# Performance work log

Measured on AMD Instinct MI355X. Metric: run time of the kernel, lower is better.

Reference implementation:

```python
import jax, jax.numpy as jnp
import numpy as np

N_NODES = 40000
N_EDGES = 640000
IN, HID, OUT = 128, 256, 47


def setup_inputs() -> dict:
    key = jax.random.key(0)
    ks = jax.random.split(key, 8)
    x = jax.random.normal(ks[0], (N_NODES, IN), dtype=jnp.float32)
    # PyTorch Linear(fan_in, fan_out): store as [fan_in, fan_out] for y = h @ W + b
    W1 = jax.random.normal(ks[1], (2 * IN, HID), dtype=jnp.float32) / np.sqrt(2 * IN)
    b1 = jnp.zeros((HID,), jnp.float32)
    W2 = jax.random.normal(ks[2], (2 * HID, HID), dtype=jnp.float32) / np.sqrt(2 * HID)
    b2 = jnp.zeros((HID,), jnp.float32)
    W3 = jax.random.normal(ks[3], (2 * HID, OUT), dtype=jnp.float32) / np.sqrt(2 * HID)
    b3 = jnp.zeros((OUT,), jnp.float32)
    src = jax.random.randint(ks[4], (N_EDGES,), 0, N_NODES, dtype=jnp.int64 if jax.config.jax_enable_x64 else jnp.int32)
    dst = jax.random.randint(ks[5], (N_EDGES,), 0, N_NODES, dtype=jnp.int64 if jax.config.jax_enable_x64 else jnp.int32)
    return {"x": x, "W1": W1, "b1": b1, "W2": W2, "b2": b2, "W3": W3, "b3": b3,
            "src": src, "dst": dst}


def _sage_layer(h, src, dst, W, b):
    # copy_u -> mean: gather src features, scatter-sum into dst, divide by in-degree
    msum = jax.ops.segment_sum(h[src], dst, num_segments=N_NODES)  # [N, d]
    deg = jax.ops.segment_sum(jnp.ones_like(dst, dtype=h.dtype), dst, num_segments=N_NODES)
    mean = msum / jnp.maximum(deg, 1.0)[:, None]  # zero-degree nodes get 0 (DGL mean convention)
    cat = jnp.concatenate([h, mean], axis=1)      # [N, 2d]
    return cat @ W + b


def reference(x, W1, b1, W2, b2, W3, b3, src, dst):
    # dropout is identity in eval mode
    h = jax.nn.relu(_sage_layer(x, src, dst, W1, b1))
    h = jax.nn.relu(_sage_layer(h, src, dst, W2, b2))
    return _sage_layer(h, src, dst, W3, b3)
```

## Files before the change

kernel.cpp:

```cpp
#include <hip/hip_runtime.h>

#define NNODES 40000
#define NEDGES 640000
#define DIN 128
#define DHID 256
#define DOUT 47
#define NCNT 40960
#define NPART (NCNT / 256)

typedef __attribute__((ext_vector_type(8))) short short8;
typedef __attribute__((ext_vector_type(4))) float f32x4;

#define GLD16(gp, lp)                                                        \
    __builtin_amdgcn_global_load_lds(                                        \
        (const __attribute__((address_space(1))) void*)(gp),                 \
        (__attribute__((address_space(3))) void*)(lp), 16, 0, 0)

__device__ inline float bf2f(unsigned short u) {
    union { unsigned int i; float f; } c; c.i = ((unsigned int)u) << 16; return c.f;
}
__device__ inline unsigned short f2bf(float f) {
    union { float f; unsigned int i; } c; c.f = f;
    unsigned int x = c.i;
    x += 0x7fff + ((x >> 16) & 1);
    return (unsigned short)(x >> 16);
}

__global__ void hist_kernel(const int* __restrict__ dst, int* __restrict__ cnt) {
    int t = blockIdx.x * blockDim.x + threadIdx.x;
    if (t < NEDGES) atomicAdd(&cnt[dst[t]], 1);
}

__global__ void part_kernel(const int* __restrict__ cnt, int* __restrict__ part) {
    int b = blockIdx.x, t = threadIdx.x;
    int v = cnt[b * 256 + t];
#pragma unroll
    for (int off = 32; off > 0; off >>= 1) v += __shfl_down(v, off);
    __shared__ int ws[4];
    if ((t & 63) == 0) ws[t >> 6] = v;
    __syncthreads();
    if (t == 0) part[b] = ws[0] + ws[1] + ws[2] + ws[3];
}

__global__ void scanpart_kernel(const int* __restrict__ part, int* __restrict__ partoff) {
    __shared__ int sh[256];
    int t = threadIdx.x;
    int v = (t < NPART) ? part[t] : 0;
    sh[t] = v;
    __syncthreads();
    for (int off = 1; off < 256; off <<= 1) {
        int add = (t >= off) ? sh[t - off] : 0;
        __syncthreads();
        sh[t] += add;
        __syncthreads();
    }
    if (t < NPART) partoff[t] = sh[t] - v;
}

__global__ void writeptr_kernel(const int* __restrict__ cnt, const int* __restrict__ partoff,
                                int* __restrict__ rowptr) {
    __shared__ int sh[256];
    int b = blockIdx.x, t = threadIdx.x;
    int idx = b * 256 + t;
    int v = cnt[idx];
    sh[t] = v;
    __syncthreads();
    for (int off = 1; off < 256; off <<= 1) {
        int add = (t >= off) ? sh[t - off] : 0;
        __syncthreads();
        sh[t] += add;
        __syncthreads();
    }
    rowptr[idx] = partoff[b] + sh[t] - v;
}

__global__ void fill_kernel(const int* __restrict__ src, const int* __restrict__ dst,
                            const int* __restrict__ rowptr, int* __restrict__ fill,
                            unsigned short* __restrict__ eidx) {
    int e = blockIdx.x * blockDim.x + threadIdx.x;
    if (e < NEDGES) {
        int d = dst[e];
        int pos = rowptr[d] + atomicAdd(&fill[d], 1);
        eidx[pos] = (unsigned short)src[e];
    }
}

__global__ void conv_all_kernel(const float* __restrict__ x,
                                const float* __restrict__ W1,
                                const float* __restrict__ W2,
                                const float* __restrict__ W3,
                                unsigned short* __restrict__ xbf,
                                unsigned short* __restrict__ wt1,
                                unsigned short* __restrict__ wt2,
                                unsigned short* __restrict__ wt3) {
    const int N0 = NNODES * DIN / 4;
    const int N1 = 2 * DIN * DHID;
    const int N2 = 2 * DHID * DHID;
    const int N3 = 94 * 256;
    int t = blockIdx.x * blockDim.x + threadIdx.x;
    if (t < N0) {
        float4 v = ((const float4*)x)[t];
        ushort4 r;
        r.x = f2bf(v.x); r.y = f2bf(v.y); r.z = f2bf(v.z); r.w = f2bf(v.w);
        ((ushort4*)xbf)[t] = r;
    } else if (t < N0 + N1) {
        int u = t - N0;
        int k = u >> 8, n = u & 255;
        wt1[(size_t)n * 256 + k] = f2bf(W1[u]);
    } else if (t < N0 + N1 + N2) {
        int u = t - N0 - N1;
        int k = u >> 8, n = u & 255;
        wt2[(size_t)n * 512 + k] = f2bf(W2[u]);
    } else if (t < N0 + N1 + N2 + N3) {
        int u = t - N0 - N1 - N2;
        int n = u >> 8, k = u & 255;
        float v = (n < 47) ? W3[(size_t)k * DOUT + n]
                           : W3[(size_t)(k + DHID) * DOUT + (n - 47)];
        wt3[u] = f2bf(v);
    }
}

template <int D>
__global__ void agg_bf16_kernel(const unsigned short* __restrict__ h,
                                const int* __restrict__ rowptr,
                                const unsigned short* __restrict__ eidx,
                                unsigned short* __restrict__ mean) {
    constexpr int VPL = D / 64;
    const int node = blockIdx.x * (blockDim.x >> 6) + (threadIdx.x >> 6);
    if (node >= NNODES) return;
    const int lane = threadIdx.x & 63;
    const int beg = rowptr[node], end = rowptr[node + 1];
    const unsigned short* hp = h + lane * VPL;

    float acc[VPL];
#pragma unroll
    for (int i = 0; i < VPL; ++i) acc[i] = 0.0f;

    for (int base = beg; base < end; base += 64) {
        int n = min(64, end - base);
        int myidx = (base + lane < end) ? (int)eidx[base + lane] : 0;
        int j = 0;
        for (; j + 8 <= n; j += 8) {
            int s[8];
#pragma unroll
            for (int u = 0; u < 8; ++u) s[u] = __shfl(myidx, j + u);
            if constexpr (VPL == 4) {
                ushort4 v[8];
#pragma unroll
                for (int u = 0; u < 8; ++u) v[u] = *(const ushort4*)(hp + (size_t)s[u] * D);
#pragma unroll
                for (int u = 0; u < 8; ++u) {
                    acc[0] += bf2f(v[u].x); acc[1] += bf2f(v[u].y);
                    acc[2] += bf2f(v[u].z); acc[3] += bf2f(v[u].w);
                }
            } else {
                ushort2 v[8];
#pragma unroll
                for (int u = 0; u < 8; ++u) v[u] = *(const ushort2*)(hp + (size_t)s[u] * D);
#pragma unroll
                for (int u = 0; u < 8; ++u) {
                    acc[0] += bf2f(v[u].x); acc[1] += bf2f(v[u].y);
                }
            }
        }
        for (; j + 4 <= n; j += 4) {
            int s[4];
#pragma unroll
            for (int u = 0; u < 4; ++u) s[u] = __shfl(myidx, j + u);
            if constexpr (VPL == 4) {
                ushort4 v[4];
#pragma unroll
                for (int u = 0; u < 4; ++u) v[u] = *(const ushort4*)(hp + (size_t)s[u] * D);
#pragma unroll
                for (int u = 0; u < 4; ++u) {
                    acc[0] += bf2f(v[u].x); acc[1] += bf2f(v[u].y);
                    acc[2] += bf2f(v[u].z); acc[3] += bf2f(v[u].w);
                }
            } else {
                ushort2 v[4];
#pragma unroll
                for (int u = 0; u < 4; ++u) v[u] = *(const ushort2*)(hp + (size_t)s[u] * D);
#pragma unroll
                for (int u = 0; u < 4; ++u) {
                    acc[0] += bf2f(v[u].x); acc[1] += bf2f(v[u].y);
                }
            }
        }
        for (; j < n; ++j) {
            int s = __shfl(myidx, j);
            if constexpr (VPL == 4) {
                ushort4 v = *(const ushort4*)(hp + (size_t)s * D);
                acc[0] += bf2f(v.x); acc[1] += bf2f(v.y);
                acc[2] += bf2f(v.z); acc[3] += bf2f(v.w);
            } else {
                ushort2 v = *(const ushort2*)(hp + (size_t)s * D);
                acc[0] += bf2f(v.x); acc[1] += bf2f(v.y);
            }
        }
    }
    float inv = (end > beg) ? 1.0f / (float)(end - beg) : 0.0f;
    unsigned short* o = mean + (size_t)node * D + lane * VPL;
    if constexpr (VPL == 4) {
        ushort4 r;
        r.x = f2bf(acc[0] * inv); r.y = f2bf(acc[1] * inv);
        r.z = f2bf(acc[2] * inv); r.w = f2bf(acc[3] * inv);
        *(ushort4*)o = r;
    } else {
        ushort2 r;
        r.x = f2bf(acc[0] * inv); r.y = f2bf(acc[1] * inv);
        *(ushort2*)o = r;
    }
}

__global__ void agg_p_kernel(const unsigned short* __restrict__ P,
                             const int* __restrict__ rowptr,
                             const unsigned short* __restrict__ eidx,
                             float* __restrict__ out) {
    const int node = blockIdx.x * (blockDim.x >> 6) + (threadIdx.x >> 6);
    if (node >= NNODES) return;
    const int lane = threadIdx.x & 63;
    const int beg = rowptr[node], end = rowptr[node + 1];
    const bool active = lane < 48;
    const int lc = active ? lane : 0;

    float acc = 0.0f;
    for (int base = beg; base < end; base += 64) {
        int n = min(64, end - base);
        int myidx = (base + lane < end) ? (int)eidx[base + lane] : 0;
        int j = 0;
        for (; j + 4 <= n; j += 4) {
            int s0 = __shfl(myidx, j);
            int s1 = __shfl(myidx, j + 1);
            int s2 = __shfl(myidx, j + 2);
            int s3 = __shfl(myidx, j + 3);
            if (active) {
                float a = bf2f(P[(size_t)s0 * 48 + lc]) + bf2f(P[(size_t)s1 * 48 + lc]);
                float b = bf2f(P[(size_t)s2 * 48 + lc]) + bf2f(P[(size_t)s3 * 48 + lc]);
                acc += a + b;
            }
        }
        for (; j < n; ++j) {
            int s = __shfl(myidx, j);
            if (active) acc += bf2f(P[(size_t)s * 48 + lc]);
        }
    }
    if (lane < 47 && end > beg) {
        out[(size_t)node * DOUT + lane] += acc / (float)(end - beg);
    }
}

template <int D>
__launch_bounds__(256, 2)
__global__ void gemm_fused_kernel(const unsigned short* __restrict__ H,
                                  const unsigned short* __restrict__ Mn,
                                  const unsigned short* __restrict__ Wt,
                                  const float* __restrict__ bias,
                                  unsigned short* __restrict__ hout) {
    constexpr int K = 2 * D;
    __shared__ uint4 As4[64 * 4];
    __shared__ uint4 Bs4[256 * 4];

    const int tid = threadIdx.x;
    const int lane = tid & 63;
    const int w = tid >> 6;
    const int row0 = blockIdx.x * 64;

    const int lr = lane >> 2;
    const int lslot = lane & 3;
    const int arow = w * 16 + lr;
    const int aoff = (lslot ^ ((arow >> 1) & 3)) * 8;
    const size_t abase = (size_t)(row0 + arow) * D;

    f32x4 acc[4][4];
#pragma unroll
    for (int m = 0; m < 4; ++m)
#pragma unroll
        for (int n = 0; n < 4; ++n) {
            f32x4 z = {0.0f, 0.0f, 0.0f, 0.0f};
            acc[m][n] = z;
        }

    const int fr = lane & 15;
    const int sl = lane >> 4;

#pragma unroll
    for (int k0 = 0; k0 < K; k0 += 32) {
        {
            const unsigned short* ap = (k0 < D) ? (H + abase + k0 + aoff)
                                                : (Mn + abase + (k0 - D) + aoff);
            GLD16(ap, (char*)As4 + w * 1024);
        }
#pragma unroll
        for (int c = 0; c < 4; ++c) {
            int q = w * 4 + c;
            int brow = q * 16 + lr;
            const unsigned short* bp =
                Wt + (size_t)brow * K + k0 + ((lslot ^ ((brow >> 1) & 3)) * 8);
            GLD16(bp, (char*)Bs4 + q * 1024);
        }
        __syncthreads();

        short8 af[4], bfv[4];
#pragma unroll
        for (int m = 0; m < 4; ++m) {
            int r = m * 16 + fr;
            union { uint4 u; short8 s; } cc;
            cc.u = As4[r * 4 + (sl ^ ((r >> 1) & 3))];
            af[m] = cc.s;
        }
#pragma unroll
        for (int n = 0; n < 4; ++n) {
            int r = w * 64 + n * 16 + fr;
            union { uint4 u; short8 s; } cc;
            cc.u = Bs4[r * 4 + (sl ^ ((r >> 1) & 3))];
            bfv[n] = cc.s;
        }
#pragma unroll
        for (int m = 0; m < 4; ++m)
#pragma unroll
            for (int n = 0; n < 4; ++n)
                acc[m][n] = __builtin_amdgcn_mfma_f32_16x16x32_bf16(af[m], bfv[n], acc[m][n], 0, 0, 0);
        __syncthreads();
    }

#pragma unroll
    for (int m = 0; m < 4; ++m) {
#pragma unroll
        for (int n = 0; n < 4; ++n) {
            int col = w * 64 + n * 16 + fr;
            float bv = bias[col];
#pragma unroll
            for (int q = 0; q < 4; ++q) {
                int row = row0 + m * 16 + sl * 4 + q;
                float v = fmaxf(acc[m][n][q] + bv, 0.0f);
                hout[(size_t)row * 256 + col] = f2bf(v);
            }
        }
    }
}

__launch_bounds__(256, 2)
__global__ void gemm3_kernel(const unsigned short* __restrict__ H,
                             const unsigned short* __restrict__ Wt,
                             const float* __restrict__ bias,
                             float* __restrict__ outp,
                             unsigned short* __restrict__ Pout,
                             int d, int N) {
    const int K = 2 * d;
    __shared__ uint4 AsB[128 * 4];
    __shared__ uint4 BsB[128 * 4];

    const int tid = threadIdx.x;
    const int lane = tid & 63;
    const int wid = tid >> 6;
    const int wr = wid >> 1, wc = wid & 1;
    const int row0 = blockIdx.x * 128;

    const int sr = tid >> 1;
    const int sh = tid & 1;
    const int gar = min(row0 + sr, NNODES - 1);
    const int gbr = min(sr, N - 1);
    const int ssw = (sr >> 1) & 3;

    f32x4 acc[4][4];
#pragma unroll
    for (int m = 0; m < 4; ++m)
#pragma unroll
        for (int n = 0; n < 4; ++n) {
            f32x4 z = {0.0f, 0.0f, 0.0f, 0.0f};
            acc[m][n] = z;
        }

    for (int k0 = 0; k0 < K; k0 += 32) {
        {
            const unsigned short* p = H + (size_t)gar * K + k0 + sh * 16;
            uint4 v0 = *(const uint4*)p;
            uint4 v1 = *(const uint4*)(p + 8);
            AsB[sr * 4 + ((2 * sh) ^ ssw)]     = v0;
            AsB[sr * 4 + ((2 * sh + 1) ^ ssw)] = v1;
        }
        {
            const unsigned short* p = Wt + (size_t)gbr * K + k0 + sh * 16;
            uint4 v0 = *(const uint4*)p;
            uint4 v1 = *(const uint4*)(p + 8);
            BsB[sr * 4 + ((2 * sh) ^ ssw)]     = v0;
            BsB[sr * 4 + ((2 * sh + 1) ^ ssw)] = v1;
        }
        __syncthreads();

        short8 af[4], bfv[4];
        const int fr = lane & 15;
        const int slot = lane >> 4;
#pragma unroll
        for (int m = 0; m < 4; ++m) {
            int r = wr * 64 + m * 16 + fr;
            union { uint4 u; short8 s; } cc;
            cc.u = AsB[r * 4 + (slot ^ ((r >> 1) & 3))];
            af[m] = cc.s;
        }
#pragma unroll
        for (int n = 0; n < 4; ++n) {
            int r = wc * 64 + n * 16 + fr;
            union { uint4 u; short8 s; } cc;
            cc.u = BsB[r * 4 + (slot ^ ((r >> 1) & 3))];
            bfv[n] = cc.s;
        }
#pragma unroll
        for (int m = 0; m < 4; ++m)
#pragma unroll
            for (int n = 0; n < 4; ++n)
                acc[m][n] = __builtin_amdgcn_mfma_f32_16x16x32_bf16(af[m], bfv[n], acc[m][n], 0, 0, 0);
        __syncthreads();
    }

#pragma unroll
    for (int m = 0; m < 4; ++m) {
#pragma unroll
        for (int n = 0; n < 4; ++n) {
            int col = wc * 64 + n * 16 + (lane & 15);
            if (col >= N) continue;
            float bv = (col < 47) ? bias[col] : 0.0f;
#pragma unroll
            for (int q = 0; q < 4; ++q) {
                int row = row0 + wr * 64 + m * 16 + (lane >> 4) * 4 + q;
                if (row < NNODES) {
                    float v = acc[m][n][q] + bv;
                    if (col < 47) outp[(size_t)row * DOUT + col] = v;
                    else Pout[(size_t)row * 48 + (col - 47)] = f2bf(v);
                }
            }
        }
    }
}

extern "C" void kernel_launch(void* const* d_in, const int* in_sizes, int n_in,
                              void* d_out, int out_size, void* d_ws, size_t ws_size,
                              hipStream_t stream) {
    const float* x  = (const float*)d_in[0];
    const float* W1 = (const float*)d_in[1];
    const float* b1 = (const float*)d_in[2];
    const float* W2 = (const float*)d_in[3];
    const float* b2 = (const float*)d_in[4];
    const float* W3 = (const float*)d_in[5];
    const float* b3 = (const float*)d_in[6];
    const int* src  = (const int*)d_in[7];
    const int* dst  = (const int*)d_in[8];
    float* out = (float*)d_out;

    int* rowptr  = (int*)d_ws;
    unsigned short* eidx = (unsigned short*)(rowptr + NCNT);
    int* cnt     = (int*)(eidx + NEDGES);
    int* fill    = cnt + NCNT;
    int* part    = fill + NCNT;
    int* partoff = part + 256;
    unsigned short* xbf  = (unsigned short*)(partoff + 256);
    unsigned short* h1   = xbf + (size_t)NNODES * DIN;
    unsigned short* h2   = h1 + (size_t)NNODES * DHID;
    unsigned short* mean = h2 + (size_t)NNODES * DHID;
    unsigned short* wt1  = mean + (size_t)NNODES * DHID;
    unsigned short* wt2  = wt1 + 2 * DIN * DHID;
    unsigned short* wt3  = wt2 + 2 * DHID * DHID;
    unsigned short* P    = mean;

    hipMemsetAsync(cnt, 0, 2 * NCNT * sizeof(int), stream);
    hist_kernel<<<(NEDGES + 255) / 256, 256, 0, stream>>>(dst, cnt);
    part_kernel<<<NPART, 256, 0, stream>>>(cnt, part);
    scanpart_kernel<<<1, 256, 0, stream>>>(part, partoff);
    writeptr_kernel<<<NPART, 256, 0, stream>>>(cnt, partoff, rowptr);
    fill_kernel<<<(NEDGES + 255) / 256, 256, 0, stream>>>(src, dst, rowptr, fill, eidx);

    {
        const int NT = NNODES * DIN / 4 + 2 * DIN * DHID + 2 * DHID * DHID + 94 * 256;
        conv_all_kernel<<<(NT + 255) / 256, 256, 0, stream>>>(x, W1, W2, W3, xbf, wt1, wt2, wt3);
    }

    agg_bf16_kernel<DIN><<<NNODES / 4, 256, 0, stream>>>(xbf, rowptr, eidx, mean);
    gemm_fused_kernel<DIN><<<NNODES / 64, 256, 0, stream>>>(xbf, mean, wt1, b1, h1);

    agg_bf16_kernel<DHID><<<NNODES / 4, 256, 0, stream>>>(h1, rowptr, eidx, mean);
    gemm_fused_kernel<DHID><<<NNODES / 64, 256, 0, stream>>>(h1, mean, wt2, b2, h2);

    gemm3_kernel<<<(NNODES + 127) / 128, 256, 0, stream>>>(h2, wt3, b3, out, P, DHID / 2, 94);
    agg_p_kernel<<<NNODES / 4, 256, 0, stream>>>(P, rowptr, eidx, out);
}
```

Measured before the change: 219.2 us.

## Slice feature aggregation by column chunks and fuse prep kernels

Replaces the per-node aggregation with a kernel that splits the feature dimension into 32-column slices across grid.x. Each wave handles one node and one slice, with four 16-lane groups processing different edges in parallel and reducing via shuffles at the end. Each slice then reads only 64 bytes per neighbour row, which should improve L2 locality for the random gathers, at the cost of reading eidx/rowptr several times and an extra cross-lane reduction. Separately, the counter memset is folded into the conversion kernel and the single-block partition scan is merged into writeptr, removing two launches.

```diff
diff --git a/kernel.cpp b/kernel.cpp
--- a/kernel.cpp
+++ b/kernel.cpp
@@ -42,25 +42,21 @@
     if (t == 0) part[b] = ws[0] + ws[1] + ws[2] + ws[3];
 }
 
-__global__ void scanpart_kernel(const int* __restrict__ part, int* __restrict__ partoff) {
+__global__ void writeptr_kernel(const int* __restrict__ cnt, const int* __restrict__ part,
+                                int* __restrict__ rowptr) {
+    __shared__ int shp[256];
     __shared__ int sh[256];
-    int t = threadIdx.x;
-    int v = (t < NPART) ? part[t] : 0;
-    sh[t] = v;
+    int b = blockIdx.x, t = threadIdx.x;
+    int pv = (t < NPART) ? part[t] : 0;
+    shp[t] = pv;
     __syncthreads();
     for (int off = 1; off < 256; off <<= 1) {
-        int add = (t >= off) ? sh[t - off] : 0;
-        __syncthreads();
-        sh[t] += add;
-        __syncthreads();
-    }
-    if (t < NPART) partoff[t] = sh[t] - v;
-}
-
-__global__ void writeptr_kernel(const int* __restrict__ cnt, const int* __restrict__ partoff,
-                                int* __restrict__ rowptr) {
-    __shared__ int sh[256];
-    int b = blockIdx.x, t = threadIdx.x;
+        int add = (t >= off) ? shp[t - off] : 0;
+        __syncthreads();
+        shp[t] += add;
+        __syncthreads();
+    }
+    int partoff = (b == 0) ? 0 : shp[b - 1];
     int idx = b * 256 + t;
     int v = cnt[idx];
     sh[t] = v;
@@ -71,7 +67,7 @@
         sh[t] += add;
         __syncthreads();
     }
-    rowptr[idx] = partoff[b] + sh[t] - v;
+    rowptr[idx] = partoff + sh[t] - v;
 }
 
 __global__ void fill_kernel(const int* __restrict__ src, const int* __restrict__ dst,
@@ -92,12 +88,14 @@
                                 unsigned short* __restrict__ xbf,
                                 unsigned short* __restrict__ wt1,
                                 unsigned short* __restrict__ wt2,
-                                unsigned short* __restrict__ wt3) {
+                                unsigned short* __restrict__ wt3,
+                                int* __restrict__ czero) {
     const int N0 = NNODES * DIN / 4;
     const int N1 = 2 * DIN * DHID;
     const int N2 = 2 * DHID * DHID;
     const int N3 = 94 * 256;
     int t = blockIdx.x * blockDim.x + threadIdx.x;
+    if (t < 2 * NCNT) czero[t] = 0;
     if (t < N0) {
         float4 v = ((const float4*)x)[t];
         ushort4 r;
@@ -121,94 +119,57 @@
 }
 
 template <int D>
-__global__ void agg_bf16_kernel(const unsigned short* __restrict__ h,
-                                const int* __restrict__ rowptr,
-                                const unsigned short* __restrict__ eidx,
-                                unsigned short* __restrict__ mean) {
-    constexpr int VPL = D / 64;
-    const int node = blockIdx.x * (blockDim.x >> 6) + (threadIdx.x >> 6);
+__global__ void agg_sliced2_kernel(const unsigned short* __restrict__ h,
+                                   const int* __restrict__ rowptr,
+                                   const unsigned short* __restrict__ eidx,
+                                   unsigned short* __restrict__ mean) {
+    const int c = blockIdx.x;
+    const int node = blockIdx.y * (blockDim.x >> 6) + (threadIdx.x >> 6);
     if (node >= NNODES) return;
     const int lane = threadIdx.x & 63;
+    const int g = lane >> 4;
+    const int f = lane & 15;
     const int beg = rowptr[node], end = rowptr[node + 1];
-    const unsigned short* hp = h + lane * VPL;
-
-    float acc[VPL];
-#pragma unroll
-    for (int i = 0; i < VPL; ++i) acc[i] = 0.0f;
-
+    const unsigned short* hp = h + c * 32 + f * 2;
+
+    float ax = 0.0f, ay = 0.0f;
     for (int base = beg; base < end; base += 64) {
         int n = min(64, end - base);
         int myidx = (base + lane < end) ? (int)eidx[base + lane] : 0;
         int j = 0;
-        for (; j + 8 <= n; j += 8) {
-            int s[8];
-#pragma unroll
-            for (int u = 0; u < 8; ++u) s[u] = __shfl(myidx, j + u);
-            if constexpr (VPL == 4) {
-                ushort4 v[8];
-#pragma unroll
-                for (int u = 0; u < 8; ++u) v[u] = *(const ushort4*)(hp + (size_t)s[u] * D);
-#pragma unroll
-                for (int u = 0; u < 8; ++u) {
-                    acc[0] += bf2f(v[u].x); acc[1] += bf2f(v[u].y);
-                    acc[2] += bf2f(v[u].z); acc[3] += bf2f(v[u].w);
-                }
-            } else {
-                ushort2 v[8];
-#pragma unroll
-                for (int u = 0; u < 8; ++u) v[u] = *(const ushort2*)(hp + (size_t)s[u] * D);
-#pragma unroll
-                for (int u = 0; u < 8; ++u) {
-                    acc[0] += bf2f(v[u].x); acc[1] += bf2f(v[u].y);
-                }
-            }
+        for (; j + 16 <= n; j += 16) {
+            int s0 = __shfl(myidx, j + g);
+            int s1 = __shfl(myidx, j + 4 + g);
+            int s2 = __shfl(myidx, j + 8 + g);
+            int s3 = __shfl(myidx, j + 12 + g);
+            ushort2 v0 = *(const ushort2*)(hp + (size_t)s0 * D);
+            ushort2 v1 = *(const ushort2*)(hp + (size_t)s1 * D);
+            ushort2 v2 = *(const ushort2*)(hp + (size_t)s2 * D);
+            ushort2 v3 = *(const ushort2*)(hp + (size_t)s3 * D);
+            ax += (bf2f(v0.x) + bf2f(v1.x)) + (bf2f(v2.x) + bf2f(v3.x));
+            ay += (bf2f(v0.y) + bf2f(v1.y)) + (bf2f(v2.y) + bf2f(v3.y));
         }
         for (; j + 4 <= n; j += 4) {
-            int s[4];
-#pragma unroll
-            for (int u = 0; u < 4; ++u) s[u] = __shfl(myidx, j + u);
-            if constexpr (VPL == 4) {
-                ushort4 v[4];
-#pragma unroll
-                for (int u = 0; u < 4; ++u) v[u] = *(const ushort4*)(hp + (size_t)s[u] * D);
-#pragma unroll
-                for (int u = 0; u < 4; ++u) {
-                    acc[0] += bf2f(v[u].x); acc[1] += bf2f(v[u].y);
-                    acc[2] += bf2f(v[u].z); acc[3] += bf2f(v[u].w);
-                }
-            } else {
-                ushort2 v[4];
-#pragma unroll
-                for (int u = 0; u < 4; ++u) v[u] = *(const ushort2*)(hp + (size_t)s[u] * D);
-#pragma unroll
-                for (int u = 0; u < 4; ++u) {
-                    acc[0] += bf2f(v[u].x); acc[1] += bf2f(v[u].y);
-                }
-            }
-        }
-        for (; j < n; ++j) {
-            int s = __shfl(myidx, j);
-            if constexpr (VPL == 4) {
-                ushort4 v = *(const ushort4*)(hp + (size_t)s * D);
-                acc[0] += bf2f(v.x); acc[1] += bf2f(v.y);
-                acc[2] += bf2f(v.z); acc[3] += bf2f(v.w);
-            } else {
-                ushort2 v = *(const ushort2*)(hp + (size_t)s * D);
-                acc[0] += bf2f(v.x); acc[1] += bf2f(v.y);
-            }
-        }
-    }
-    float inv = (end > beg) ? 1.0f / (float)(end - beg) : 0.0f;
-    unsigned short* o = mean + (size_t)node * D + lane * VPL;
-    if constexpr (VPL == 4) {
-        ushort4 r;
-        r.x = f2bf(acc[0] * inv); r.y = f2bf(acc[1] * inv);
-        r.z = f2bf(acc[2] * inv); r.w = f2bf(acc[3] * inv);
-        *(ushort4*)o = r;
-    } else {
-        ushort2 r;
-        r.x = f2bf(acc[0] * inv); r.y = f2bf(acc[1] * inv);
-        *(ushort2*)o = r;
+            int s0 = __shfl(myidx, j + g);
+            ushort2 v0 = *(const ushort2*)(hp + (size_t)s0 * D);
+            ax += bf2f(v0.x);
+            ay += bf2f(v0.y);
+        }
+        int rem = n - j;
+        int srcl = (g < rem) ? (j + g) : 0;
+        int s0 = __shfl(myidx, srcl);
+        if (g < rem) {
+            ushort2 v0 = *(const ushort2*)(hp + (size_t)s0 * D);
+            ax += bf2f(v0.x);
+            ay += bf2f(v0.y);
+        }
+    }
+    ax += __shfl_xor(ax, 16); ay += __shfl_xor(ay, 16);
+    ax += __shfl_xor(ax, 32); ay += __shfl_xor(ay, 32);
+    if (lane < 16) {
+        float inv = (end > beg) ? 1.0f / (float)(end - beg) : 0.0f;
+        unsigned int rv = (unsigned int)f2bf(ax * inv) | ((unsigned int)f2bf(ay * inv) << 16);
+        __builtin_nontemporal_store(rv, (unsigned int*)(mean + (size_t)node * D + c * 32) + f);
     }
 }
 
@@ -452,8 +413,7 @@
     int* cnt     = (int*)(eidx + NEDGES);
     int* fill    = cnt + NCNT;
     int* part    = fill + NCNT;
-    int* partoff = part + 256;
-    unsigned short* xbf  = (unsigned short*)(partoff + 256);
+    unsigned short* xbf  = (unsigned short*)(part + 256);
     unsigned short* h1   = xbf + (size_t)NNODES * DIN;
     unsigned short* h2   = h1 + (size_t)NNODES * DHID;
     unsigned short* mean = h2 + (size_t)NNODES * DHID;
@@ -462,22 +422,26 @@
     unsigned short* wt3  = wt2 + 2 * DHID * DHID;
     unsigned short* P    = mean;
 
-    hipMemsetAsync(cnt, 0, 2 * NCNT * sizeof(int), stream);
+    {
+        const int NT = NNODES * DIN / 4 + 2 * DIN * DHID + 2 * DHID * DHID + 94 * 256;
+        conv_all_kernel<<<(NT + 255) / 256, 256, 0, stream>>>(x, W1, W2, W3, xbf, wt1, wt2, wt3, cnt);
+    }
+
     hist_kernel<<<(NEDGES + 255) / 256, 256, 0, stream>>>(dst, cnt);
     part_kernel<<<NPART, 256, 0, stream>>>(cnt, part);
-    scanpart_kernel<<<1, 256, 0, stream>>>(part, partoff);
-    writeptr_kernel<<<NPART, 256, 0, stream>>>(cnt, partoff, rowptr);
+    writeptr_kernel<<<NPART, 256, 0, stream>>>(cnt, part, rowptr);
     fill_kernel<<<(NEDGES + 255) / 256, 256, 0, stream>>>(src, dst, rowptr, fill, eidx);
 
     {
-        const int NT = NNODES * DIN / 4 + 2 * DIN * DHID + 2 * DHID * DHID + 94 * 256;
-        conv_all_kernel<<<(NT + 255) / 256, 256, 0, stream>>>(x, W1, W2, W3, xbf, wt1, wt2, wt3);
-    }
-
-    agg_bf16_kernel<DIN><<<NNODES / 4, 256, 0, stream>>>(xbf, rowptr, eidx, mean);
+        dim3 grid(DIN / 32, (NNODES + 15) / 16);
+        agg_sliced2_kernel<DIN><<<grid, 1024, 0, stream>>>(xbf, rowptr, eidx, mean);
+    }
     gemm_fused_kernel<DIN><<<NNODES / 64, 256, 0, stream>>>(xbf, mean, wt1, b1, h1);
 
-    agg_bf16_kernel<DHID><<<NNODES / 4, 256, 0, stream>>>(h1, rowptr, eidx, mean);
+    {
+        dim3 grid(DHID / 32, (NNODES + 15) / 16);
+        agg_sliced2_kernel<DHID><<<grid, 1024, 0, stream>>>(h1, rowptr, eidx, mean);
+    }
     gemm_fused_kernel<DHID><<<NNODES / 64, 256, 0, stream>>>(h1, mean, wt2, b2, h2);
 
     gemm3_kernel<<<(NNODES + 127) / 128, 256, 0, stream>>>(h2, wt3, b3, out, P, DHID / 2, 94);
```

Result: slower. 316.6 us (+44.5%).

## Double-buffer GEMM LDS tiles and fold scan/memset into existing kernels

Applied to the files above, without the earlier changes.

The fused GEMM kernel now double-buffers its A and B LDS tiles, issuing the global-to-LDS loads for the next K slice before computing the current one, with one barrier per iteration instead of two. The separate partition-scan kernel is folded into writeptr, where every block redundantly scans the partition sums. The count memset is folded into the conversion kernel, which now runs first. Together these cut launch count and try to hide load latency in the GEMM, at the cost of doubled LDS use (which may lower occupancy) and redundant per-block scan work.

```diff
diff --git a/kernel.cpp b/kernel.cpp
--- a/kernel.cpp
+++ b/kernel.cpp
@@ -42,25 +42,21 @@
     if (t == 0) part[b] = ws[0] + ws[1] + ws[2] + ws[3];
 }
 
-__global__ void scanpart_kernel(const int* __restrict__ part, int* __restrict__ partoff) {
+__global__ void writeptr_kernel(const int* __restrict__ cnt, const int* __restrict__ part,
+                                int* __restrict__ rowptr) {
+    __shared__ int shp[256];
     __shared__ int sh[256];
-    int t = threadIdx.x;
-    int v = (t < NPART) ? part[t] : 0;
-    sh[t] = v;
+    int b = blockIdx.x, t = threadIdx.x;
+    int pv = (t < NPART) ? part[t] : 0;
+    shp[t] = pv;
     __syncthreads();
     for (int off = 1; off < 256; off <<= 1) {
-        int add = (t >= off) ? sh[t - off] : 0;
-        __syncthreads();
-        sh[t] += add;
-        __syncthreads();
-    }
-    if (t < NPART) partoff[t] = sh[t] - v;
-}
-
-__global__ void writeptr_kernel(const int* __restrict__ cnt, const int* __restrict__ partoff,
-                                int* __restrict__ rowptr) {
-    __shared__ int sh[256];
-    int b = blockIdx.x, t = threadIdx.x;
+        int add = (t >= off) ? shp[t - off] : 0;
+        __syncthreads();
+        shp[t] += add;
+        __syncthreads();
+    }
+    int partoff = (b == 0) ? 0 : shp[b - 1];
     int idx = b * 256 + t;
     int v = cnt[idx];
     sh[t] = v;
@@ -71,7 +67,7 @@
         sh[t] += add;
         __syncthreads();
     }
-    rowptr[idx] = partoff[b] + sh[t] - v;
+    rowptr[idx] = partoff + sh[t] - v;
 }
 
 __global__ void fill_kernel(const int* __restrict__ src, const int* __restrict__ dst,
@@ -92,12 +88,14 @@
                                 unsigned short* __restrict__ xbf,
                                 unsigned short* __restrict__ wt1,
                                 unsigned short* __restrict__ wt2,
-                                unsigned short* __restrict__ wt3) {
+                                unsigned short* __restrict__ wt3,
+                                int* __restrict__ czero) {
     const int N0 = NNODES * DIN / 4;
     const int N1 = 2 * DIN * DHID;
     const int N2 = 2 * DHID * DHID;
     const int N3 = 94 * 256;
     int t = blockIdx.x * blockDim.x + threadIdx.x;
+    if (t < 2 * NCNT) czero[t] = 0;
     if (t < N0) {
         float4 v = ((const float4*)x)[t];
         ushort4 r;
@@ -257,8 +255,9 @@
                                   const float* __restrict__ bias,
                                   unsigned short* __restrict__ hout) {
     constexpr int K = 2 * D;
-    __shared__ uint4 As4[64 * 4];
-    __shared__ uint4 Bs4[256 * 4];
+    constexpr int NK = K / 32;
+    __shared__ uint4 As4[2][64 * 4];
+    __shared__ uint4 Bs4[2][256 * 4];
 
     const int tid = threadIdx.x;
     const int lane = tid & 63;
@@ -267,8 +266,8 @@
 
     const int lr = lane >> 2;
     const int lslot = lane & 3;
+    const int swz = (lslot ^ ((lr >> 1) & 3)) * 8;
     const int arow = w * 16 + lr;
-    const int aoff = (lslot ^ ((arow >> 1) & 3)) * 8;
     const size_t abase = (size_t)(row0 + arow) * D;
 
     f32x4 acc[4][4];
@@ -283,36 +282,45 @@
     const int fr = lane & 15;
     const int sl = lane >> 4;
 
-#pragma unroll
-    for (int k0 = 0; k0 < K; k0 += 32) {
-        {
-            const unsigned short* ap = (k0 < D) ? (H + abase + k0 + aoff)
-                                                : (Mn + abase + (k0 - D) + aoff);
-            GLD16(ap, (char*)As4 + w * 1024);
-        }
+    {
+        GLD16(H + abase + swz, (char*)As4[0] + w * 1024);
 #pragma unroll
         for (int c = 0; c < 4; ++c) {
-            int q = w * 4 + c;
-            int brow = q * 16 + lr;
-            const unsigned short* bp =
-                Wt + (size_t)brow * K + k0 + ((lslot ^ ((brow >> 1) & 3)) * 8);
-            GLD16(bp, (char*)Bs4 + q * 1024);
-        }
-        __syncthreads();
+            int brow = (w * 4 + c) * 16 + lr;
+            GLD16(Wt + (size_t)brow * K + swz, (char*)Bs4[0] + (w * 4 + c) * 1024);
+        }
+    }
+    __syncthreads();
+
+#pragma unroll
+    for (int t = 0; t < NK; ++t) {
+        const int cur = t & 1;
+        if (t + 1 < NK) {
+            const int k0 = (t + 1) * 32;
+            const unsigned short* ap = (k0 < D) ? (H + abase + k0 + swz)
+                                                : (Mn + abase + (k0 - D) + swz);
+            GLD16(ap, (char*)As4[cur ^ 1] + w * 1024);
+#pragma unroll
+            for (int c = 0; c < 4; ++c) {
+                int brow = (w * 4 + c) * 16 + lr;
+                GLD16(Wt + (size_t)brow * K + k0 + swz,
+                      (char*)Bs4[cur ^ 1] + (w * 4 + c) * 1024);
+            }
+        }
 
         short8 af[4], bfv[4];
 #pragma unroll
         for (int m = 0; m < 4; ++m) {
             int r = m * 16 + fr;
             union { uint4 u; short8 s; } cc;
-            cc.u = As4[r * 4 + (sl ^ ((r >> 1) & 3))];
+            cc.u = As4[cur][r * 4 + (sl ^ ((r >> 1) & 3))];
             af[m] = cc.s;
         }
 #pragma unroll
         for (int n = 0; n < 4; ++n) {
             int r = w * 64 + n * 16 + fr;
             union { uint4 u; short8 s; } cc;
-            cc.u = Bs4[r * 4 + (sl ^ ((r >> 1) & 3))];
+            cc.u = Bs4[cur][r * 4 + (sl ^ ((r >> 1) & 3))];
             bfv[n] = cc.s;
         }
 #pragma unroll
@@ -320,6 +328,7 @@
 #pragma unroll
             for (int n = 0; n < 4; ++n)
                 acc[m][n] = __builtin_amdgcn_mfma_f32_16x16x32_bf16(af[m], bfv[n], acc[m][n], 0, 0, 0);
+
         __syncthreads();
     }
 
@@ -452,8 +461,7 @@
     int* cnt     = (int*)(eidx + NEDGES);
     int* fill    = cnt + NCNT;
     int* part    = fill + NCNT;
-    int* partoff = part + 256;
-    unsigned short* xbf  = (unsigned short*)(partoff + 256);
+    unsigned short* xbf  = (unsigned short*)(part + 256);
     unsigned short* h1   = xbf + (size_t)NNODES * DIN;
     unsigned short* h2   = h1 + (size_t)NNODES * DHID;
     unsigned short* mean = h2 + (size_t)NNODES * DHID;
@@ -462,17 +470,15 @@
     unsigned short* wt3  = wt2 + 2 * DHID * DHID;
     unsigned short* P    = mean;
 
-    hipMemsetAsync(cnt, 0, 2 * NCNT * sizeof(int), stream);
+    {
+        const int NT = NNODES * DIN / 4 + 2 * DIN * DHID + 2 * DHID * DHID + 94 * 256;
+        conv_all_kernel<<<(NT + 255) / 256, 256, 0, stream>>>(x, W1, W2, W3, xbf, wt1, wt2, wt3, cnt);
+    }
+
     hist_kernel<<<(NEDGES + 255) / 256, 256, 0, stream>>>(dst, cnt);
     part_kernel<<<NPART, 256, 0, stream>>>(cnt, part);
-    scanpart_kernel<<<1, 256, 0, stream>>>(part, partoff);
-    writeptr_kernel<<<NPART, 256, 0, stream>>>(cnt, partoff, rowptr);
+    writeptr_kernel<<<NPART, 256, 0, stream>>>(cnt, part, rowptr);
     fill_kernel<<<(NEDGES + 255) / 256, 256, 0, stream>>>(src, dst, rowptr, fill, eidx);
-
-    {
-        const int NT = NNODES * DIN / 4 + 2 * DIN * DHID + 2 * DHID * DHID + 94 * 256;
-        conv_all_kernel<<<(NT + 255) / 256, 256, 0, stream>>>(x, W1, W2, W3, xbf, wt1, wt2, wt3);
-    }
 
     agg_bf16_kernel<DIN><<<NNODES / 4, 256, 0, stream>>>(xbf, rowptr, eidx, mean);
     gemm_fused_kernel<DIN><<<NNODES / 64, 256, 0, stream>>>(xbf, mean, wt1, b1, h1);
```

Measured after the change: 215.2 us. No clear change (-1.8%).
